# Kernel optimization log

Measured on AMD Instinct MI355X. Metric: run time of the kernel, lower is better.

The kernel has to match this reference:

```python
import jax, jax.numpy as jnp
import numpy as np

NUM_HEADS = 16
THETA = 10000.0


def _apply_rope(x, pos):
    # x: [b, h, t, d_k], pos: [t] int
    d = x.shape[-1]
    inv_freq = THETA ** (-jnp.arange(0, d, 2, dtype=jnp.float32) / d)  # [d/2]
    ang = pos.astype(jnp.float32)[:, None] * inv_freq                  # [t, d/2]
    cos, sin = jnp.cos(ang), jnp.sin(ang)
    x1, x2 = x[..., ::2], x[..., 1::2]
    r1 = x1 * cos - x2 * sin
    r2 = x1 * sin + x2 * cos
    return jnp.stack([r1, r2], axis=-1).reshape(x.shape)


def setup_inputs() -> dict:
    key = jax.random.key(0)
    k1, k2, k3 = jax.random.split(key, 3)
    b, t, dm = 4, 2048, 2048
    in_features = jax.random.normal(k1, (b, t, dm), dtype=jnp.float32)
    token_positions = jnp.arange(t, dtype=jnp.int64)
    W_qkv = jax.random.normal(k2, (3 * dm, dm), dtype=jnp.float32) * 0.02
    W_o = jax.random.normal(k3, (dm, dm), dtype=jnp.float32) * 0.02
    return {"in_features": in_features, "token_positions": token_positions,
            "W_qkv": W_qkv, "W_o": W_o}


def reference(in_features, token_positions, W_qkv, W_o):
    b, t, dm = in_features.shape
    h = NUM_HEADS
    dk = dm // h
    # fused QKV projection (Linear: y = x W^T)
    qkv = in_features @ W_qkv.T                       # [b, t, 3*dm]
    q, k, v = jnp.split(qkv, 3, axis=-1)
    def to_heads(x):
        return x.reshape(b, t, h, dk).transpose(0, 2, 1, 3)  # [b, h, t, dk]
    q, k, v = to_heads(q), to_heads(k), to_heads(v)
    q = _apply_rope(q, token_positions)
    k = _apply_rope(k, token_positions)
    # causal SDPA
    scale = 1.0 / np.sqrt(dk).astype(np.float32)
    scores = jnp.einsum('bhqd,bhkd->bhqk', q, k) * scale
    causal = jnp.tril(jnp.ones((t, t), dtype=bool))
    scores = jnp.where(causal, scores, jnp.finfo(scores.dtype).min)
    attn = jax.nn.softmax(scores, axis=-1)
    out = jnp.einsum('bhqk,bhkd->bhqd', attn, v)      # [b, h, t, dk]
    out = out.transpose(0, 2, 1, 3).reshape(b, t, dm)
    return out @ W_o.T
```

## Files before the change

### kernel.cpp

```cpp
#include <hip/hip_runtime.h>

typedef unsigned short u16;
typedef __attribute__((ext_vector_type(8))) short s8v;
typedef __attribute__((ext_vector_type(8))) __bf16 bf8;
typedef __attribute__((ext_vector_type(4))) float f4v;

#define GLB(p) ((const __attribute__((address_space(1))) void*)(p))
#define LDS(p) ((__attribute__((address_space(3))) void*)(p))

static __device__ __forceinline__ float b2f(u16 u) {
    union { unsigned int i; float f; } v; v.i = ((unsigned int)u) << 16; return v.f;
}
static __device__ __forceinline__ u16 f2b(float f) {
    union { float f; unsigned int i; } v; v.f = f;
    v.i += 0x7fffu + ((v.i >> 16) & 1u);
    return (u16)(v.i >> 16);
}

__global__ __launch_bounds__(256) void k_conv(const float* __restrict__ X,
                                              const float* __restrict__ Wq,
                                              const float* __restrict__ Wo,
                                              u16* __restrict__ Xb,
                                              u16* __restrict__ Wqb,
                                              u16* __restrict__ Wob) {
    int i = blockIdx.x * 256 + threadIdx.x;
    const float* in; u16* out; int off;
    if (i < 4194304)      { in = X;  out = Xb;  off = i; }
    else if (i < 7340032) { in = Wq; out = Wqb; off = i - 4194304; }
    else                  { in = Wo; out = Wob; off = i - 7340032; }
    float4 v = ((const float4*)in)[off];
    union { u16 u[4]; unsigned long long ll; } o;
    o.u[0] = f2b(v.x); o.u[1] = f2b(v.y); o.u[2] = f2b(v.z); o.u[3] = f2b(v.w);
    ((unsigned long long*)out)[off] = o.ll;
}

template<int MODE>
__global__ __launch_bounds__(512, 2) void k_gemm_bt(
    const u16* __restrict__ A, const u16* __restrict__ B,
    int K, int N, int gx,
    u16* __restrict__ Qb, u16* __restrict__ Kb, u16* __restrict__ Vt,
    float* __restrict__ Cf, const int* __restrict__ pos)
{
    extern __shared__ __align__(16) u16 Ls[];

    const int t    = threadIdx.x;
    const int lane = t & 63;
    const int wid  = t >> 6;
    const int wm = wid >> 2, wn = wid & 3;
    const int la = lane & 15, lb = lane >> 4;

    const int bid = (int)blockIdx.x;
    const int id2 = (bid & 7) * ((int)gridDim.x >> 3) + (bid >> 3);
    const int bx = id2 % gx, by = id2 / gx;
    const long arow0 = (long)by * 256;
    const long brow0 = (long)bx * 256;

    const int sr = t >> 3;
    const int sg = (t & 7) ^ (sr & 7);
    const u16* Asrc = A + (arow0 + sr) * (long)K + sg * 8;
    const u16* Bsrc = B + (brow0 + sr) * (long)K + sg * 8;
    const long K64 = 64 * (long)K, K128 = 128 * (long)K;
    u16* ldst = Ls + t * 8;

#define STG(q_, op_, h_, kt_) do {                                              \
        const u16* s_ = ((op_) ? Bsrc : Asrc) + (h_) * K128 + (long)(kt_) * 64; \
        u16* d_ = ldst + (q_) * 32768 + (op_) * 16384 + (h_) * 8192;            \
        __builtin_amdgcn_global_load_lds(GLB(s_),       LDS(d_),        16, 0, 0); \
        __builtin_amdgcn_global_load_lds(GLB(s_ + K64), LDS(d_ + 4096), 16, 0, 0); \
    } while (0)
#define RD(off) (*(const bf8*)(Ls + (off)))

    f4v acc[8][4];
#pragma unroll
    for (int m = 0; m < 8; m++)
#pragma unroll
        for (int n = 0; n < 4; n++) acc[m][n] = (f4v){0.f, 0.f, 0.f, 0.f};

    const int r7 = la & 7;
    const int gA0 = (lb ^ r7) * 8;
    const int gA1 = ((lb ^ r7) ^ 4) * 8;
    const int aRow = wm * 8192 + la * 64;
    const int bRow = 16384 + (wn >> 1) * 8192 + ((wn & 1) * 64 + la) * 64;

    const int NKT = K >> 6;
    STG(0, 0, 0, 0); STG(0, 0, 1, 0); STG(0, 1, 0, 0); STG(0, 1, 1, 0);

    for (int X = 0; X < NKT; ++X) {
        asm volatile("s_waitcnt vmcnt(0)" ::: "memory");
        __builtin_amdgcn_s_barrier();
        if (X + 1 < NKT) {
            const int q = (X + 1) & 1;
            STG(q, 0, 0, X + 1); STG(q, 0, 1, X + 1);
            STG(q, 1, 0, X + 1); STG(q, 1, 1, X + 1);
        }

        const int D = (X & 1) << 15;
        bf8 aF[8][2], bF[4][2];
#pragma unroll
        for (int mi = 0; mi < 8; mi++) aF[mi][0] = RD(D + aRow + mi * 1024 + gA0);
#pragma unroll
        for (int ni = 0; ni < 4; ni++) bF[ni][0] = RD(D + bRow + ni * 1024 + gA0);
#pragma unroll
        for (int mi = 0; mi < 8; mi++) aF[mi][1] = RD(D + aRow + mi * 1024 + gA1);
#pragma unroll
        for (int ni = 0; ni < 4; ni++) bF[ni][1] = RD(D + bRow + ni * 1024 + gA1);

        __builtin_amdgcn_s_setprio(1);
#pragma unroll
        for (int kk = 0; kk < 2; kk++)
#pragma unroll
            for (int mi = 0; mi < 8; mi++)
#pragma unroll
                for (int ni = 0; ni < 4; ni++)
                    acc[mi][ni] = __builtin_amdgcn_mfma_f32_16x16x32_bf16(aF[mi][kk], bF[ni][kk], acc[mi][ni], 0, 0, 0);
        __builtin_amdgcn_s_setprio(0);
    }
    asm volatile("s_waitcnt vmcnt(0)" ::: "memory");
#undef STG
#undef RD

    if (MODE == 1) {
#pragma unroll
        for (int mi = 0; mi < 8; mi++)
#pragma unroll
            for (int ni = 0; ni < 4; ni++) {
                const long grow0 = arow0 + wm * 128 + mi * 16 + lb * 4;
                const int  gcol  = (int)brow0 + wn * 64 + ni * 16 + la;
#pragma unroll
                for (int i = 0; i < 4; i++)
                    Cf[(grow0 + i) * (long)N + gcol] = acc[mi][ni][i];
            }
        return;
    }

    __syncthreads();
    const int part = (int)(brow0 >> 11);
    const int colp = (int)brow0 & 2047;
    const int h0   = colp >> 7;
    const int bidx = (int)(arow0 >> 11);
    const int t0   = (int)arow0 & 2047;

    if (part == 2) {
#pragma unroll
        for (int mi = 0; mi < 8; mi++)
#pragma unroll
            for (int ni = 0; ni < 4; ni++) {
                const int tlb = wm * 128 + mi * 16 + lb * 4;
                const int dl  = wn * 64 + ni * 16 + la;
#pragma unroll
                for (int i2 = 0; i2 < 2; i2++) {
                    unsigned int pk = (unsigned int)f2b(acc[mi][ni][i2 * 2])
                                    | ((unsigned int)f2b(acc[mi][ni][i2 * 2 + 1]) << 16);
                    *(unsigned int*)(Ls + dl * 264 + tlb + i2 * 2) = pk;
                }
            }
        __syncthreads();
#pragma unroll
        for (int j = 0; j < 16; j++) {
            const int dl = j * 16 + wid * 2 + (lane >> 5);
            const int c  = lane & 31;
            bf8 v = *(const bf8*)(Ls + dl * 264 + c * 8);
            const long bh = (long)(bidx * 16 + h0 + (dl >> 7));
            *(bf8*)(Vt + (bh << 18) + ((long)(dl & 127) << 11) + t0 + c * 8) = v;
        }
    } else {
        u16* dst = (part == 0) ? Qb : Kb;
#pragma unroll
        for (int mi = 0; mi < 8; mi++)
#pragma unroll
            for (int ni = 0; ni < 4; ni++) {
                const int tlb = wm * 128 + mi * 16 + lb * 4;
                const int dl  = wn * 64 + ni * 16 + la;
#pragma unroll
                for (int i = 0; i < 4; i++)
                    Ls[(tlb + i) * 264 + dl] = f2b(acc[mi][ni][i]);
            }
        __syncthreads();
        const int c = t & 15;
        float invf[4];
#pragma unroll
        for (int p2 = 0; p2 < 4; p2++)
            invf[p2] = exp2f((float)(c * 4 + p2) * -0.20762050593046014f);
#pragma unroll
        for (int j = 0; j < 16; j++) {
            const int R  = j * 32 + (t >> 4);
            const int tl = R >> 1, hh = R & 1;
            s8v v = *(const s8v*)(Ls + tl * 264 + hh * 128 + c * 8);
            const float pf = (float)pos[t0 + tl];
            union { u16 u[8]; s8v v; } ov;
#pragma unroll
            for (int p2 = 0; p2 < 4; p2++) {
                float x1 = b2f((u16)v[2 * p2]);
                float x2 = b2f((u16)v[2 * p2 + 1]);
                float sn, cs;
                __sincosf(pf * invf[p2], &sn, &cs);
                ov.u[2 * p2]     = f2b(x1 * cs - x2 * sn);
                ov.u[2 * p2 + 1] = f2b(x1 * sn + x2 * cs);
            }
            const long bh = (long)(bidx * 16 + h0 + hh);
            *(s8v*)(dst + ((bh << 11) + t0 + tl) * 128 + c * 8) = ov.v;
        }
    }
}

__global__ __launch_bounds__(256) void k_attn(const u16* __restrict__ Qb,
                                              const u16* __restrict__ Kb,
                                              const u16* __restrict__ Vt,
                                              u16* __restrict__ Ob)
{
    extern __shared__ __align__(16) u16 Sm[];
    u16* KsD = Sm;
    u16* VsD = Sm + 16384;
    u16* PlD = Sm + 32768;

    const int tid  = threadIdx.x;
    const int lane = tid & 63;
    const int w    = tid >> 6;
    const int la = lane & 15, lb = lane >> 4;
    const int qg = 15 - ((int)blockIdx.x >> 6);
    const int bh = blockIdx.x & 63;
    const long base = (long)bh << 18;
    const int qt = qg * 4 + w;
    const int q0 = qt * 32;
    const int n32 = qt + 1;
    const int NT = qg * 2 + 2;
    const float scale = 0.08838834764831845f;

    bf8 qf[2][4];
#pragma unroll
    for (int m = 0; m < 2; m++)
#pragma unroll
        for (int kb = 0; kb < 4; kb++)
            qf[m][kb] = *(const bf8*)(Qb + base + (long)(q0 + m * 16 + la) * 128 + kb * 32 + lb * 8);

    f4v o[2][8];
#pragma unroll
    for (int m = 0; m < 2; m++)
#pragma unroll
        for (int n = 0; n < 8; n++) o[m][n] = (f4v){0.f, 0.f, 0.f, 0.f};
    float lst[2][4];
#pragma unroll
    for (int m = 0; m < 2; m++)
#pragma unroll
        for (int i = 0; i < 4; i++) lst[m][i] = 0.f;

    char* Pb = (char*)(PlD + w * 1024);

    const int krow = tid >> 4;
    const int kgr  = (tid & 15) ^ (krow & 7);
    const int vrow = tid >> 3;
    const int vgr  = (tid & 7) ^ (vrow & 7);

#define STAGE(buf, jt_) do {                                                         \
        const int kv0_ = (jt_) * 64;                                                \
        _Pragma("unroll")                                                           \
        for (int i_ = 0; i_ < 4; i_++) {                                            \
            __builtin_amdgcn_global_load_lds(                                       \
                GLB(Kb + base + (long)(kv0_ + i_ * 16 + krow) * 128 + kgr * 8),     \
                LDS(KsD + (buf) * 8192 + i_ * 2048 + tid * 8), 16, 0, 0);           \
            __builtin_amdgcn_global_load_lds(                                       \
                GLB(Vt + base + (long)(i_ * 32 + vrow) * 2048 + kv0_ + vgr * 8),    \
                LDS(VsD + (buf) * 8192 + i_ * 2048 + tid * 8), 16, 0, 0);           \
        }                                                                           \
    } while (0)

    STAGE(0, 0);

    for (int jt = 0; jt < NT; ++jt) {
        const int buf = jt & 1;
        asm volatile("s_waitcnt vmcnt(0)" ::: "memory");
        __builtin_amdgcn_s_barrier();
        if (jt + 1 < NT) STAGE(buf ^ 1, jt + 1);

        const u16* KsB = KsD + buf * 8192;
        const u16* VsB = VsD + buf * 8192;

#pragma unroll
        for (int h = 0; h < 2; h++) {
            const int j32 = jt * 2 + h;
            if (j32 < n32) {
                f4v s[2][2];
                s[0][0] = s[0][1] = s[1][0] = s[1][1] = (f4v){0.f, 0.f, 0.f, 0.f};
#pragma unroll
                for (int n = 0; n < 2; n++) {
                    const int rr = h * 32 + n * 16 + la;
#pragma unroll
                    for (int kb = 0; kb < 4; kb++) {
                        bf8 kf = *(const bf8*)(KsB + rr * 128 + (((kb * 4 + lb) ^ (la & 7)) * 8));
                        s[0][n] = __builtin_amdgcn_mfma_f32_16x16x32_bf16(qf[0][kb], kf, s[0][n], 0, 0, 0);
                        s[1][n] = __builtin_amdgcn_mfma_f32_16x16x32_bf16(qf[1][kb], kf, s[1][n], 0, 0, 0);
                    }
                }

                bf8 vf[8];
#pragma unroll
                for (int nO = 0; nO < 8; nO++) {
                    const int rv = nO * 16 + la;
                    vf[nO] = *(const bf8*)(VsB + rv * 64 + (((h * 4 + lb) ^ (la & 7)) * 8));
                }

                const bool diag = (j32 == qt);
                float p[2][2][4];
#pragma unroll
                for (int m = 0; m < 2; m++)
#pragma unroll
                    for (int n = 0; n < 2; n++)
#pragma unroll
                        for (int i = 0; i < 4; i++) {
                            float v = __expf(fmaf(s[m][n][i], scale, -8.0f));
                            if (diag && (n * 16 + la) > (m * 16 + lb * 4 + i)) v = 0.f;
                            p[m][n][i] = v;
                            lst[m][i] += v;
                        }

#pragma unroll
                for (int m = 0; m < 2; m++)
#pragma unroll
                    for (int n = 0; n < 2; n++)
#pragma unroll
                        for (int i = 0; i < 4; i++) {
                            const int row = m * 16 + lb * 4 + i;
                            const int colb = (n * 16 + la) * 2;
                            *(u16*)(Pb + row * 64 + (colb ^ ((row & 3) << 4))) = f2b(p[m][n][i]);
                        }
                bf8 pa[2];
#pragma unroll
                for (int am = 0; am < 2; am++) {
                    const int row = am * 16 + la;
                    pa[am] = *(const bf8*)(Pb + row * 64 + ((lb * 16) ^ ((row & 3) << 4)));
                }
#pragma unroll
                for (int nO = 0; nO < 8; nO++) {
                    o[0][nO] = __builtin_amdgcn_mfma_f32_16x16x32_bf16(pa[0], vf[nO], o[0][nO], 0, 0, 0);
                    o[1][nO] = __builtin_amdgcn_mfma_f32_16x16x32_bf16(pa[1], vf[nO], o[1][nO], 0, 0, 0);
                }
            }
        }
    }
#undef STAGE

    float linv[2][4];
#pragma unroll
    for (int m = 0; m < 2; m++)
#pragma unroll
        for (int i = 0; i < 4; i++) {
            float l = lst[m][i];
            l += __shfl_xor(l, 1);
            l += __shfl_xor(l, 2);
            l += __shfl_xor(l, 4);
            l += __shfl_xor(l, 8);
            linv[m][i] = 1.0f / l;
        }

    const int b = bh >> 4, h = bh & 15;
#pragma unroll
    for (int m = 0; m < 2; m++)
#pragma unroll
        for (int nO = 0; nO < 8; nO++)
#pragma unroll
            for (int i = 0; i < 4; i++) {
                const int row = q0 + m * 16 + lb * 4 + i;
                const int d = nO * 16 + la;
                Ob[((long)(b * 2048 + row) << 11) + h * 128 + d] = f2b(o[m][nO][i] * linv[m][i]);
            }
}

extern "C" void kernel_launch(void* const* d_in, const int* in_sizes, int n_in,
                              void* d_out, int out_size, void* d_ws, size_t ws_size,
                              hipStream_t stream)
{
    const float* X    = (const float*)d_in[0];
    const int*   pos  = (const int*)d_in[1];
    const float* Wqkv = (const float*)d_in[2];
    const float* Wo   = (const float*)d_in[3];
    float* out = (float*)d_out;

    char* ws = (char*)d_ws;
    u16* Xb    = (u16*)(ws + 0);
    u16* Wqkvb = (u16*)(ws + 33554432);
    u16* Wob   = (u16*)(ws + 58720256);
    u16* Qb    = (u16*)(ws + 67108864);
    u16* Kb    = (u16*)(ws + 100663296);
    u16* Vt    = (u16*)(ws + 134217728);
    u16* Ob    = (u16*)(ws + 167772160);

    k_conv<<<32768, 256, 0, stream>>>(X, Wqkv, Wo, Xb, Wqkvb, Wob);
    k_gemm_bt<0><<<768, 512, 135168, stream>>>(Xb, Wqkvb, 2048, 6144, 24, Qb, Kb, Vt, nullptr, pos);
    k_attn<<<1024, 256, 73728, stream>>>(Qb, Kb, Vt, Ob);
    k_gemm_bt<1><<<256, 512, 131072, stream>>>(Ob, Wob, 2048, 2048, 8, nullptr, nullptr, nullptr, out, nullptr);
}
```

Before: 393.7 us.

## Deepen GEMM LDS pipeline to four stages with K=32 tiles and split compute phases

The GEMM main loop moves from a double-buffered K=64 tile to a four-stage ring of K=32 tiles. The LDS layout and swizzle are rearranged, and each iteration is split into two half-M MFMA phases interleaved with A and B prefetches and partial vmcnt waits. The aim is to hide global-to-LDS load latency behind MFMA work rather than draining all loads before every tile. In exchange there are more barriers per K step and half as much MFMA work between them, and the prefetch index clamping at the tail reloads the last tile redundantly.

```diff
diff --git a/kernel.cpp b/kernel.cpp
--- a/kernel.cpp
+++ b/kernel.cpp
@@ -55,18 +55,27 @@
     const long arow0 = (long)by * 256;
     const long brow0 = (long)bx * 256;
 
-    const int sr = t >> 3;
-    const int sg = (t & 7) ^ (sr & 7);
-    const u16* Asrc = A + (arow0 + sr) * (long)K + sg * 8;
-    const u16* Bsrc = B + (brow0 + sr) * (long)K + sg * 8;
-    const long K64 = 64 * (long)K, K128 = 128 * (long)K;
+    const int r0 = t >> 3, sl = t & 7;
+    const int sA0 = sl ^ (r0 & 7);
+    const long RA0 = r0 + 128 * (sA0 >> 2);
+    const long RA1 = 64 + r0 + 128 * (sA0 >> 2);
+    const u16* As0 = A + (arow0 + RA0) * (long)K + (sA0 & 3) * 8;
+    const u16* As1 = A + (arow0 + RA1) * (long)K + (sA0 & 3) * 8;
+    const u16* Bs0 = B + (brow0 + RA0) * (long)K + (sA0 & 3) * 8;
+    const u16* Bs1 = B + (brow0 + RA1) * (long)K + (sA0 & 3) * 8;
     u16* ldst = Ls + t * 8;
 
-#define STG(q_, op_, h_, kt_) do {                                              \
-        const u16* s_ = ((op_) ? Bsrc : Asrc) + (h_) * K128 + (long)(kt_) * 64; \
-        u16* d_ = ldst + (q_) * 32768 + (op_) * 16384 + (h_) * 8192;            \
-        __builtin_amdgcn_global_load_lds(GLB(s_),       LDS(d_),        16, 0, 0); \
-        __builtin_amdgcn_global_load_lds(GLB(s_ + K64), LDS(d_ + 4096), 16, 0, 0); \
+#define STGA(s_, kt_) do {                                                        \
+        const long ko_ = (long)(kt_) * 32;                                        \
+        u16* d_ = ldst + (s_) * 16384;                                            \
+        __builtin_amdgcn_global_load_lds(GLB(As0 + ko_), LDS(d_),        16, 0, 0); \
+        __builtin_amdgcn_global_load_lds(GLB(As1 + ko_), LDS(d_ + 4096), 16, 0, 0); \
+    } while (0)
+#define STGB(s_, kt_) do {                                                        \
+        const long ko_ = (long)(kt_) * 32;                                        \
+        u16* d_ = ldst + (s_) * 16384 + 8192;                                     \
+        __builtin_amdgcn_global_load_lds(GLB(Bs0 + ko_), LDS(d_),        16, 0, 0); \
+        __builtin_amdgcn_global_load_lds(GLB(Bs1 + ko_), LDS(d_ + 4096), 16, 0, 0); \
     } while (0)
 #define RD(off) (*(const bf8*)(Ls + (off)))
 
@@ -76,47 +85,52 @@
 #pragma unroll
         for (int n = 0; n < 4; n++) acc[m][n] = (f4v){0.f, 0.f, 0.f, 0.f};
 
-    const int r7 = la & 7;
-    const int gA0 = (lb ^ r7) * 8;
-    const int gA1 = ((lb ^ r7) ^ 4) * 8;
-    const int aRow = wm * 8192 + la * 64;
-    const int bRow = 16384 + (wn >> 1) * 8192 + ((wn & 1) * 64 + la) * 64;
-
-    const int NKT = K >> 6;
-    STG(0, 0, 0, 0); STG(0, 0, 1, 0); STG(0, 1, 0, 0); STG(0, 1, 1, 0);
+    const int aOff = la * 64 + ((lb + 4 * wm) ^ (la & 7)) * 8;
+    const int bOff = 8192 + ((wn & 1) * 64 + la) * 64 + ((lb + 4 * (wn >> 1)) ^ (la & 7)) * 8;
+
+    const int NKT = K >> 5;
+    STGA(0, 0); STGB(0, 0); STGA(1, 1); STGB(1, 1); STGA(2, 2); STGB(2, 2);
+    asm volatile("s_waitcnt vmcnt(8)" ::: "memory");
+    __builtin_amdgcn_s_barrier();
 
     for (int X = 0; X < NKT; ++X) {
-        asm volatile("s_waitcnt vmcnt(0)" ::: "memory");
+        const int D  = (X & 3) * 16384;
+        const int s3 = ((X + 3) & 3);
+        const int S  = (X + 3 < NKT) ? X + 3 : NKT - 1;
+        bf8 aE[4], bF[4], aO[4];
+
+#pragma unroll
+        for (int mi = 0; mi < 4; mi++) aE[mi] = RD(D + aOff + mi * 1024);
+#pragma unroll
+        for (int ni = 0; ni < 4; ni++) bF[ni] = RD(D + bOff + ni * 1024);
+        STGA(s3, S);
+        asm volatile("s_waitcnt vmcnt(6)" ::: "memory");
         __builtin_amdgcn_s_barrier();
-        if (X + 1 < NKT) {
-            const int q = (X + 1) & 1;
-            STG(q, 0, 0, X + 1); STG(q, 0, 1, X + 1);
-            STG(q, 1, 0, X + 1); STG(q, 1, 1, X + 1);
-        }
-
-        const int D = (X & 1) << 15;
-        bf8 aF[8][2], bF[4][2];
-#pragma unroll
-        for (int mi = 0; mi < 8; mi++) aF[mi][0] = RD(D + aRow + mi * 1024 + gA0);
-#pragma unroll
-        for (int ni = 0; ni < 4; ni++) bF[ni][0] = RD(D + bRow + ni * 1024 + gA0);
-#pragma unroll
-        for (int mi = 0; mi < 8; mi++) aF[mi][1] = RD(D + aRow + mi * 1024 + gA1);
-#pragma unroll
-        for (int ni = 0; ni < 4; ni++) bF[ni][1] = RD(D + bRow + ni * 1024 + gA1);
-
         __builtin_amdgcn_s_setprio(1);
 #pragma unroll
-        for (int kk = 0; kk < 2; kk++)
-#pragma unroll
-            for (int mi = 0; mi < 8; mi++)
-#pragma unroll
-                for (int ni = 0; ni < 4; ni++)
-                    acc[mi][ni] = __builtin_amdgcn_mfma_f32_16x16x32_bf16(aF[mi][kk], bF[ni][kk], acc[mi][ni], 0, 0, 0);
+        for (int mi = 0; mi < 4; mi++)
+#pragma unroll
+            for (int ni = 0; ni < 4; ni++)
+                acc[mi][ni] = __builtin_amdgcn_mfma_f32_16x16x32_bf16(aE[mi], bF[ni], acc[mi][ni], 0, 0, 0);
         __builtin_amdgcn_s_setprio(0);
+        __builtin_amdgcn_s_barrier();
+
+#pragma unroll
+        for (int mi = 0; mi < 4; mi++) aO[mi] = RD(D + aOff + (4 + mi) * 1024);
+        STGB(s3, S);
+        __builtin_amdgcn_s_barrier();
+        __builtin_amdgcn_s_setprio(1);
+#pragma unroll
+        for (int mi = 0; mi < 4; mi++)
+#pragma unroll
+            for (int ni = 0; ni < 4; ni++)
+                acc[4 + mi][ni] = __builtin_amdgcn_mfma_f32_16x16x32_bf16(aO[mi], bF[ni], acc[4 + mi][ni], 0, 0, 0);
+        __builtin_amdgcn_s_setprio(0);
+        __builtin_amdgcn_s_barrier();
     }
     asm volatile("s_waitcnt vmcnt(0)" ::: "memory");
-#undef STG
+#undef STGA
+#undef STGB
 #undef RD
 
     if (MODE == 1) {
```

New measurement: 411.2 us. +4.5%, slower.
